# Optimization experiments

Hardware: AMD Instinct MI355X
Metric: run time of the kernel (lower is better)

Reference implementation:

```python
import math
import jax, jax.numpy as jnp
import numpy as np

DIM = 2048
NUM_HEADS = 16
HEAD_DIM = 128
SEQ = 2048
BATCH = 2
HIDDEN = 5632  # round_up(int(4*2048*2/3), 256)
EPS = 1e-6


def setup_inputs() -> dict:
    key = jax.random.key(0)
    ks = jax.random.split(key, 8)
    s = 0.02
    x = jax.random.normal(ks[0], (BATCH, SEQ, DIM), jnp.float32)
    wq = jax.random.normal(ks[1], (DIM, NUM_HEADS * HEAD_DIM), jnp.float32) * s
    wk = jax.random.normal(ks[2], (DIM, NUM_HEADS * HEAD_DIM), jnp.float32) * s
    wv = jax.random.normal(ks[3], (DIM, NUM_HEADS * HEAD_DIM), jnp.float32) * s
    wo = jax.random.normal(ks[4], (NUM_HEADS * HEAD_DIM, DIM), jnp.float32) * s
    w_mlp = jax.random.normal(ks[5], (HIDDEN, DIM), jnp.float32) * s
    v_mlp = jax.random.normal(ks[6], (HIDDEN, DIM), jnp.float32) * s
    w2_mlp = jax.random.normal(ks[7], (DIM, HIDDEN), jnp.float32) * s
    norm1_w = jnp.ones((DIM,), jnp.float32)
    norm2_w = jnp.ones((DIM,), jnp.float32)
    # RoPE tables: theta_i = 10000^{-2i/head_dim}, angle[p,i] = p * theta_i
    inv_freq = 1.0 / (10000.0 ** (np.arange(0, HEAD_DIM, 2, dtype=np.float32) / HEAD_DIM))
    angles = np.arange(SEQ, dtype=np.float32)[:, None] * inv_freq[None, :]  # [S, D/2]
    freqs_cos = jnp.asarray(np.cos(angles))
    freqs_sin = jnp.asarray(np.sin(angles))
    return {"x": x, "wq": wq, "wk": wk, "wv": wv, "wo": wo,
            "w_mlp": w_mlp, "v_mlp": v_mlp, "w2_mlp": w2_mlp,
            "norm1_w": norm1_w, "norm2_w": norm2_w,
            "freqs_cos": freqs_cos, "freqs_sin": freqs_sin}


def _rope(t, cos, sin):
    # t: [B,S,H,D] -> pairs, complex multiply by (cos + i sin)
    B, S, H, D = t.shape
    t = t.reshape(B, S, H, D // 2, 2)
    x0, x1 = t[..., 0], t[..., 1]
    c = cos[None, :S, None, :]
    s = sin[None, :S, None, :]
    o0 = x0 * c - x1 * s
    o1 = x0 * s + x1 * c
    return jnp.stack([o0, o1], axis=-1).reshape(B, S, H, D)


def _rmsnorm(x, w):
    x = x * jax.lax.rsqrt(jnp.mean(x * x, axis=-1, keepdims=True) + EPS)
    return w * x


def _attention(x, wq, wk, wv, wo, cos, sin):
    B, S, _ = x.shape
    q = (x @ wq).reshape(B, S, NUM_HEADS, HEAD_DIM)
    k = (x @ wk).reshape(B, S, NUM_HEADS, HEAD_DIM)
    v = (x @ wv).reshape(B, S, NUM_HEADS, HEAD_DIM)
    q = _rope(q, cos, sin)
    k = _rope(k, cos, sin)
    scores = jnp.einsum('bqhd,bkhd->bhqk', q, k) / math.sqrt(HEAD_DIM)
    causal = jnp.tril(jnp.ones((S, S), bool))
    scores = jnp.where(causal[None, None], scores, -jnp.inf)
    probs = jax.nn.softmax(scores.astype(jnp.float32), axis=-1)
    o = jnp.einsum('bhqk,bkhd->bqhd', probs, v).reshape(B, S, NUM_HEADS * HEAD_DIM)
    return o @ wo


def _mlp(x, w, v, w2):
    return (jax.nn.silu(x @ w.T) * (x @ v.T)) @ w2.T


def reference(x, wq, wk, wv, wo, w_mlp, v_mlp, w2_mlp, norm1_w, norm2_w, freqs_cos, freqs_sin):
    x = x + _attention(x, wq, wk, wv, wo, freqs_cos, freqs_sin)
    x = _rmsnorm(x, norm1_w)
    x = x + _mlp(x, w_mlp, v_mlp, w2_mlp)
    x = _rmsnorm(x, norm2_w)
    return x
```

## Files before the change

### kernel.cpp

```cpp
#include <hip/hip_runtime.h>

typedef unsigned short u16;
typedef unsigned int u32;
typedef float f32x4 __attribute__((ext_vector_type(4)));
typedef short bf16x8 __attribute__((ext_vector_type(8)));

#define DIM 2048
#define SEQ 2048
#define NHEAD 16
#define HDIM 128
#define BATCH 2
#define HIDDEN 5632
#define ROWS 4096

__device__ __forceinline__ float b2f(u16 h) { return __uint_as_float(((u32)h) << 16); }
__device__ __forceinline__ u16 f2b(float f) {
  u32 u = __float_as_uint(f);
  return (u16)((u + 0x7fffu + ((u >> 16) & 1u)) >> 16);
}

__global__ __launch_bounds__(256) void cvt_f2b(const float* __restrict__ in, u16* __restrict__ out, int n) {
  int i = (blockIdx.x * 256 + threadIdx.x) * 4;
  if (i < n) {
    float4 v = *(const float4*)(in + i);
    u32 p0 = (u32)f2b(v.x) | ((u32)f2b(v.y) << 16);
    u32 p1 = (u32)f2b(v.z) | ((u32)f2b(v.w) << 16);
    *(uint2*)(out + i) = make_uint2(p0, p1);
  }
}

__global__ __launch_bounds__(256) void cvtT(const float* __restrict__ in, u16* __restrict__ out,
                                            int Rr, int Cc) {
  __shared__ float t[32][33];
  int tx = threadIdx.x & 31, ty = threadIdx.x >> 5;
  int r0 = blockIdx.y * 32, c0 = blockIdx.x * 32;
#pragma unroll
  for (int rr = 0; rr < 4; ++rr)
    t[ty + rr * 8][tx] = in[(size_t)(r0 + ty + rr * 8) * Cc + c0 + tx];
  __syncthreads();
#pragma unroll
  for (int rr = 0; rr < 4; ++rr)
    out[(size_t)(c0 + ty + rr * 8) * Rr + r0 + tx] = f2b(t[tx][ty + rr * 8]);
}

__device__ __forceinline__ void stage_tile(u16* lds, const u16* __restrict__ g,
                                           int row0, int col0, int ld, int wave, int lane) {
#pragma unroll
  for (int j = 0; j < 2; ++j) {
    int i = wave * 2 + j;
    const u16* gp = g + (size_t)(row0 + i * 16 + (lane >> 2)) * ld + col0 + (lane & 3) * 8;
    __builtin_amdgcn_global_load_lds((const __attribute__((address_space(1))) void*)gp,
                                     (__attribute__((address_space(3))) void*)(lds + i * 512),
                                     16, 0, 0);
  }
}

template <int EPI>
__global__ __launch_bounds__(256) void gemm_bt(const u16* __restrict__ A, const u16* __restrict__ Bt,
                                               const void* R_, void* C_, int M, int N, int K) {
  __shared__ u16 lA[2][4096];
  __shared__ u16 lB[2][4096];
  const int tid = threadIdx.x, lane = tid & 63, wave = tid >> 6;
  const int wm = wave >> 1, wn = wave & 1;
  const int gx = gridDim.x;
  const int nwg = gx * gridDim.y;
  const int id = blockIdx.y * gx + blockIdx.x;
  const int cpx = nwg >> 3;
  const int sw = (id & 7) * cpx + (id >> 3);
  const int m0 = (sw / gx) * 128, n0 = (sw % gx) * 128;
  const int rl = lane & 15, g = lane >> 4;

  stage_tile(lA[0], A, m0, 0, K, wave, lane);
  stage_tile(lB[0], Bt, n0, 0, K, wave, lane);

  f32x4 acc[4][4];
#pragma unroll
  for (int a = 0; a < 4; ++a)
#pragma unroll
    for (int b = 0; b < 4; ++b) acc[a][b] = (f32x4){0.f, 0.f, 0.f, 0.f};

  __syncthreads();

  const int nk = K / 32;
  for (int kt = 0; kt < nk; ++kt) {
    const int cur = kt & 1;
    if (kt + 1 < nk) {
      stage_tile(lA[cur ^ 1], A, m0, (kt + 1) * 32, K, wave, lane);
      stage_tile(lB[cur ^ 1], Bt, n0, (kt + 1) * 32, K, wave, lane);
    }
    bf16x8 af[4], bfr[4];
#pragma unroll
    for (int mi = 0; mi < 4; ++mi)
      af[mi] = *reinterpret_cast<const bf16x8*>(&lA[cur][(wm * 64 + mi * 16 + rl) * 32 + g * 8]);
#pragma unroll
    for (int ni = 0; ni < 4; ++ni)
      bfr[ni] = *reinterpret_cast<const bf16x8*>(&lB[cur][(wn * 64 + ni * 16 + rl) * 32 + g * 8]);
#pragma unroll
    for (int mi = 0; mi < 4; ++mi)
#pragma unroll
      for (int ni = 0; ni < 4; ++ni)
        acc[mi][ni] = __builtin_amdgcn_mfma_f32_16x16x32_bf16(af[mi], bfr[ni], acc[mi][ni], 0, 0, 0);
    __syncthreads();
  }

#pragma unroll
  for (int mi = 0; mi < 4; ++mi)
#pragma unroll
    for (int ni = 0; ni < 4; ++ni)
#pragma unroll
      for (int j = 0; j < 4; ++j) {
        size_t row = m0 + wm * 64 + mi * 16 + g * 4 + j;
        size_t col = n0 + wn * 64 + ni * 16 + rl;
        size_t idx = row * N + col;
        float v = acc[mi][ni][j];
        if (EPI == 0) {
          ((u16*)C_)[idx] = f2b(v);
        } else if (EPI == 1) {
          ((float*)C_)[idx] = v + ((const float*)R_)[idx];
        } else if (EPI == 2) {
          float av = b2f(((const u16*)R_)[idx]);
          ((u16*)C_)[idx] = f2b(v * av / (1.f + __expf(-av)));
        } else if (EPI == 3) {
          ((float*)C_)[idx] = v + b2f(((const u16*)R_)[idx]);
        } else {
          size_t di = (col >> 11) * (size_t)(ROWS * (size_t)DIM) + row * DIM + (col & (DIM - 1));
          ((u16*)C_)[di] = f2b(v);
        }
      }
}

__global__ __launch_bounds__(256) void vtrans(const u16* __restrict__ V, u16* __restrict__ Vt) {
  __shared__ u16 t[32][33];
  int tx = threadIdx.x & 31, ty = threadIdx.x >> 5;
  int s0 = blockIdx.x * 32, d0 = blockIdx.y * 32;
  int bh = blockIdx.z, b = bh >> 4, h = bh & 15;
#pragma unroll
  for (int rr = 0; rr < 4; ++rr)
    t[ty + rr * 8][tx] = V[(size_t)(b * SEQ + s0 + ty + rr * 8) * DIM + h * HDIM + d0 + tx];
  __syncthreads();
#pragma unroll
  for (int rr = 0; rr < 4; ++rr)
    Vt[(size_t)(bh * HDIM + d0 + ty + rr * 8) * SEQ + s0 + tx] = t[tx][ty + rr * 8];
}

__global__ __launch_bounds__(256) void rope_kernel(u16* __restrict__ Q, u16* __restrict__ Kv,
                                                   const float* __restrict__ Cz, const float* __restrict__ Sz) {
  int t = blockIdx.x * 256 + threadIdx.x;
  int i = t & 63;
  int hh = (t >> 6) & 15;
  int row = t >> 10;
  int s = row & (SEQ - 1);
  float c = Cz[s * 64 + i], sn = Sz[s * 64 + i];
  size_t off = (size_t)row * DIM + hh * HDIM + 2 * i;
  const float sc = 0.08838834764831843f;

  u32 qp = *(const u32*)(Q + off);
  float q0 = b2f((u16)qp), q1 = b2f((u16)(qp >> 16));
  float o0 = (q0 * c - q1 * sn) * sc, o1 = (q0 * sn + q1 * c) * sc;
  *(u32*)(Q + off) = (u32)f2b(o0) | ((u32)f2b(o1) << 16);

  u32 kp = *(const u32*)(Kv + off);
  float k0 = b2f((u16)kp), k1 = b2f((u16)(kp >> 16));
  o0 = k0 * c - k1 * sn; o1 = k0 * sn + k1 * c;
  *(u32*)(Kv + off) = (u32)f2b(o0) | ((u32)f2b(o1) << 16);
}

__device__ __forceinline__ void stage_K(u16* lk, const u16* __restrict__ Kg,
                                        int b, int h, int t, int w, int lane) {
  const int r4 = lane >> 2;
  const int gsw = (lane & 3) ^ (r4 & 3);
#pragma unroll
  for (int j = 0; j < 4; ++j) {
    const u16* gp = Kg + (size_t)(b * SEQ + t * 64 + j * 16 + r4) * DIM +
                    h * HDIM + w * 32 + gsw * 8;
    __builtin_amdgcn_global_load_lds((const __attribute__((address_space(1))) void*)gp,
                                     (__attribute__((address_space(3))) void*)(lk + w * 2048 + j * 512),
                                     16, 0, 0);
  }
}

__device__ __forceinline__ void stage_V(u16* lv, const u16* __restrict__ Vg,
                                        int bh, int t, int w, int lane) {
  const int r4 = lane >> 2;
  const int gsw = (lane & 3) ^ (r4 & 3);
#pragma unroll
  for (int j = 0; j < 4; ++j) {
    int id = w * 4 + j, kc2 = id >> 3, rg = id & 7;
    const u16* gp = Vg + (size_t)(bh * HDIM + rg * 16 + r4) * SEQ +
                    t * 64 + kc2 * 32 + gsw * 8;
    __builtin_amdgcn_global_load_lds((const __attribute__((address_space(1))) void*)gp,
                                     (__attribute__((address_space(3))) void*)(lv + kc2 * 4096 + rg * 512),
                                     16, 0, 0);
  }
}

__global__ __launch_bounds__(256, 3) void attn_kernel(const u16* __restrict__ Q, const u16* __restrict__ Kp,
                                                      const u16* __restrict__ Vt, u16* __restrict__ O) {
  const int lane = threadIdx.x & 63;
  const int w = threadIdx.x >> 6;
  const int id = blockIdx.y * 32 + blockIdx.x;
  const int sw = (id & 7) * 128 + (id >> 3);
  const int qt = sw & 31;
  const int bh = sw >> 5;
  const int b = bh >> 4, h = bh & 15;
  const int rl = lane & 15, g = lane >> 4;
  const int gx8 = (g ^ (rl & 3)) * 8;

  __shared__ u16 lK[8192];
  __shared__ u16 lV[8192];
  __shared__ u16 plds[4][16][72];

  const size_t qrow = (size_t)b * SEQ + qt * 64 + w * 16;
  bf16x8 qf[4];
#pragma unroll
  for (int kc = 0; kc < 4; ++kc)
    qf[kc] = *reinterpret_cast<const bf16x8*>(Q + (qrow + rl) * DIM + h * HDIM + kc * 32 + g * 8);

  float m[4], l[4];
  f32x4 oacc[8];
#pragma unroll
  for (int j = 0; j < 4; ++j) { m[j] = -1e30f; l[j] = 0.f; }
#pragma unroll
  for (int dt = 0; dt < 8; ++dt) oacc[dt] = (f32x4){0.f, 0.f, 0.f, 0.f};

  const int qg0 = qt * 64 + w * 16 + g * 4;
  const int tmax = qt;

  stage_K(lK, Kp, b, h, 0, w, lane);
  stage_V(lV, Vt, bh, 0, w, lane);

  for (int t = 0; t <= tmax; ++t) {
    asm volatile("s_waitcnt vmcnt(4)" ::: "memory");
    __builtin_amdgcn_s_barrier();
    __builtin_amdgcn_sched_barrier(0);

    f32x4 s[4];
#pragma unroll
    for (int ct = 0; ct < 4; ++ct) s[ct] = (f32x4){0.f, 0.f, 0.f, 0.f};
#pragma unroll
    for (int ct = 0; ct < 4; ++ct)
#pragma unroll
      for (int kc = 0; kc < 4; ++kc) {
        bf16x8 kf = *reinterpret_cast<const bf16x8*>(&lK[kc * 2048 + (ct * 16 + rl) * 32 + gx8]);
        s[ct] = __builtin_amdgcn_mfma_f32_16x16x32_bf16(qf[kc], kf, s[ct], 0, 0, 0);
      }
    asm volatile("s_waitcnt lgkmcnt(0)" ::: "memory");
    __builtin_amdgcn_sched_barrier(0);
    __builtin_amdgcn_s_barrier();

    if (t < tmax) stage_K(lK, Kp, b, h, t + 1, w, lane);

    if (t < tmax) asm volatile("s_waitcnt vmcnt(4)" ::: "memory");
    else          asm volatile("s_waitcnt vmcnt(0)" ::: "memory");
    __builtin_amdgcn_s_barrier();
    __builtin_amdgcn_sched_barrier(0);

    if (t == qt) {
#pragma unroll
      for (int ct = 0; ct < 4; ++ct) {
        int kg = t * 64 + ct * 16 + rl;
#pragma unroll
        for (int j = 0; j < 4; ++j)
          if (kg > qg0 + j) s[ct][j] = -1e30f;
      }
    }
    float mx[4], al[4];
#pragma unroll
    for (int j = 0; j < 4; ++j)
      mx[j] = fmaxf(fmaxf(s[0][j], s[1][j]), fmaxf(s[2][j], s[3][j]));
#pragma unroll
    for (int off = 1; off < 16; off <<= 1)
#pragma unroll
      for (int j = 0; j < 4; ++j) mx[j] = fmaxf(mx[j], __shfl_xor(mx[j], off));
#pragma unroll
    for (int j = 0; j < 4; ++j) {
      float mn = fmaxf(m[j], mx[j]);
      al[j] = __expf(m[j] - mn);
      m[j] = mn;
    }
    float rs[4] = {0.f, 0.f, 0.f, 0.f};
#pragma unroll
    for (int ct = 0; ct < 4; ++ct)
#pragma unroll
      for (int j = 0; j < 4; ++j) {
        float p = __expf(s[ct][j] - m[j]);
        s[ct][j] = p;
        rs[j] += p;
      }
#pragma unroll
    for (int off = 1; off < 16; off <<= 1)
#pragma unroll
      for (int j = 0; j < 4; ++j) rs[j] += __shfl_xor(rs[j], off);
#pragma unroll
    for (int j = 0; j < 4; ++j) l[j] = l[j] * al[j] + rs[j];
#pragma unroll
    for (int dt = 0; dt < 8; ++dt)
#pragma unroll
      for (int j = 0; j < 4; ++j) oacc[dt][j] *= al[j];

#pragma unroll
    for (int ct = 0; ct < 4; ++ct)
#pragma unroll
      for (int j = 0; j < 4; ++j) plds[w][g * 4 + j][ct * 16 + rl] = f2b(s[ct][j]);

    bf16x8 pa[2];
#pragma unroll
    for (int kc2 = 0; kc2 < 2; ++kc2)
      pa[kc2] = *reinterpret_cast<const bf16x8*>(&plds[w][rl][kc2 * 32 + g * 8]);

#pragma unroll
    for (int dt = 0; dt < 8; ++dt)
#pragma unroll
      for (int kc2 = 0; kc2 < 2; ++kc2) {
        bf16x8 vf = *reinterpret_cast<const bf16x8*>(&lV[kc2 * 4096 + (dt * 16 + rl) * 32 + gx8]);
        oacc[dt] = __builtin_amdgcn_mfma_f32_16x16x32_bf16(pa[kc2], vf, oacc[dt], 0, 0, 0);
      }

    asm volatile("s_waitcnt lgkmcnt(0)" ::: "memory");
    __builtin_amdgcn_sched_barrier(0);
    __builtin_amdgcn_s_barrier();

    if (t < tmax) stage_V(lV, Vt, bh, t + 1, w, lane);
  }

  float inv[4];
#pragma unroll
  for (int j = 0; j < 4; ++j) inv[j] = 1.f / l[j];
#pragma unroll
  for (int dt = 0; dt < 8; ++dt)
#pragma unroll
    for (int j = 0; j < 4; ++j)
      O[(qrow + g * 4 + j) * DIM + h * HDIM + dt * 16 + rl] = f2b(oacc[dt][j] * inv[j]);
}

__global__ __launch_bounds__(256) void rmsnorm_to_bf16(const float* __restrict__ X, const float* __restrict__ W,
                                                       u16* __restrict__ O) {
  int row = blockIdx.x, tid = threadIdx.x;
  const float* xr = X + (size_t)row * DIM + tid * 8;
  float4 a = *(const float4*)xr;
  float4 bq = *(const float4*)(xr + 4);
  float v[8] = {a.x, a.y, a.z, a.w, bq.x, bq.y, bq.z, bq.w};
  float ss = 0.f;
#pragma unroll
  for (int j = 0; j < 8; ++j) ss += v[j] * v[j];
#pragma unroll
  for (int off = 32; off; off >>= 1) ss += __shfl_xor(ss, off);
  __shared__ float wss[4];
  int wave = tid >> 6, lane = tid & 63;
  if (lane == 0) wss[wave] = ss;
  __syncthreads();
  float r = rsqrtf((wss[0] + wss[1] + wss[2] + wss[3]) * (1.f / DIM) + 1e-6f);
  float4 wa = *(const float4*)(W + tid * 8);
  float4 wb = *(const float4*)(W + tid * 8 + 4);
  float wv[8] = {wa.x, wa.y, wa.z, wa.w, wb.x, wb.y, wb.z, wb.w};
  uint4 ou;
  ou.x = (u32)f2b(v[0] * r * wv[0]) | ((u32)f2b(v[1] * r * wv[1]) << 16);
  ou.y = (u32)f2b(v[2] * r * wv[2]) | ((u32)f2b(v[3] * r * wv[3]) << 16);
  ou.z = (u32)f2b(v[4] * r * wv[4]) | ((u32)f2b(v[5] * r * wv[5]) << 16);
  ou.w = (u32)f2b(v[6] * r * wv[6]) | ((u32)f2b(v[7] * r * wv[7]) << 16);
  *(uint4*)(O + (size_t)row * DIM + tid * 8) = ou;
}

__global__ __launch_bounds__(256) void rmsnorm_to_f32(const float* __restrict__ X, const float* __restrict__ W,
                                                      float* __restrict__ O) {
  int row = blockIdx.x, tid = threadIdx.x;
  const float* xr = X + (size_t)row * DIM + tid * 8;
  float4 a = *(const float4*)xr;
  float4 bq = *(const float4*)(xr + 4);
  float v[8] = {a.x, a.y, a.z, a.w, bq.x, bq.y, bq.z, bq.w};
  float ss = 0.f;
#pragma unroll
  for (int j = 0; j < 8; ++j) ss += v[j] * v[j];
#pragma unroll
  for (int off = 32; off; off >>= 1) ss += __shfl_xor(ss, off);
  __shared__ float wss[4];
  int wave = tid >> 6, lane = tid & 63;
  if (lane == 0) wss[wave] = ss;
  __syncthreads();
  float r = rsqrtf((wss[0] + wss[1] + wss[2] + wss[3]) * (1.f / DIM) + 1e-6f);
  float4 wa = *(const float4*)(W + tid * 8);
  float4 wb = *(const float4*)(W + tid * 8 + 4);
  float wv[8] = {wa.x, wa.y, wa.z, wa.w, wb.x, wb.y, wb.z, wb.w};
  float4 o0 = {v[0] * r * wv[0], v[1] * r * wv[1], v[2] * r * wv[2], v[3] * r * wv[3]};
  float4 o1 = {v[4] * r * wv[4], v[5] * r * wv[5], v[6] * r * wv[6], v[7] * r * wv[7]};
  *(float4*)(O + (size_t)row * DIM + tid * 8) = o0;
  *(float4*)(O + (size_t)row * DIM + tid * 8 + 4) = o1;
}

extern "C" void kernel_launch(void* const* d_in, const int* in_sizes, int n_in,
                              void* d_out, int out_size, void* d_ws, size_t ws_size,
                              hipStream_t stream) {
  const float* x     = (const float*)d_in[0];
  const float* wq    = (const float*)d_in[1];
  const float* wk    = (const float*)d_in[2];
  const float* wv    = (const float*)d_in[3];
  const float* wo    = (const float*)d_in[4];
  const float* w_mlp = (const float*)d_in[5];
  const float* v_mlp = (const float*)d_in[6];
  const float* w2    = (const float*)d_in[7];
  const float* n1w   = (const float*)d_in[8];
  const float* n2w   = (const float*)d_in[9];
  const float* fcos  = (const float*)d_in[10];
  const float* fsin  = (const float*)d_in[11];

  u16* ws = (u16*)d_ws;
  const size_t SZ = (size_t)ROWS * DIM;
  const size_t DD = (size_t)DIM * DIM;
  const size_t DH = (size_t)DIM * HIDDEN;

  u16* xb  = ws;
  u16* q   = ws + SZ;
  u16* k   = ws + 2 * SZ;
  u16* v   = ws + 3 * SZ;
  u16* vt  = ws + 4 * SZ;
  u16* hb  = ws + 5 * SZ;
  u16* W   = ws + 6 * SZ;
  u16* wqT = W;
  u16* wkT = W + DD;
  u16* wvT = W + 2 * DD;
  u16* woT = W + 3 * DD;
  u16* wmb = W;
  u16* vmb = W + DH;
  u16* w2b = W;
  float* x1f = (float*)ws;
  float* x2f = (float*)ws;
  u16* ba  = ws + 2 * SZ;

  dim3 blk(256);

  cvt_f2b<<<(int)(SZ / 4 / 256), blk, 0, stream>>>(x, xb, (int)SZ);
  dim3 gT(DIM / 32, DIM / 32);
  cvtT<<<gT, blk, 0, stream>>>(wq, wqT, DIM, DIM);
  cvtT<<<gT, blk, 0, stream>>>(wk, wkT, DIM, DIM);
  cvtT<<<gT, blk, 0, stream>>>(wv, wvT, DIM, DIM);
  cvtT<<<gT, blk, 0, stream>>>(wo, woT, DIM, DIM);

  dim3 gQKV(3 * DIM / 128, ROWS / 128);
  gemm_bt<4><<<gQKV, blk, 0, stream>>>(xb, W, nullptr, q, ROWS, 3 * DIM, DIM);

  cvt_f2b<<<(int)(DH / 4 / 256), blk, 0, stream>>>(w_mlp, wmb, (int)DH);

  rope_kernel<<<(ROWS * NHEAD * 64) / 256, blk, 0, stream>>>(q, k, fcos, fsin);
  vtrans<<<dim3(SEQ / 32, HDIM / 32, BATCH * NHEAD), blk, 0, stream>>>(v, vt);

  attn_kernel<<<dim3(SEQ / 64, BATCH * NHEAD), blk, 0, stream>>>(q, k, vt, v);

  dim3 gP(DIM / 128, ROWS / 128);
  gemm_bt<1><<<gP, blk, 0, stream>>>(v, woT, x, x1f, ROWS, DIM, DIM);

  cvt_f2b<<<(int)(DH / 4 / 256), blk, 0, stream>>>(v_mlp, vmb, (int)DH);

  rmsnorm_to_bf16<<<ROWS, blk, 0, stream>>>(x1f, n1w, hb);

  dim3 gM1(HIDDEN / 128, ROWS / 128);
  gemm_bt<0><<<gM1, blk, 0, stream>>>(hb, wmb, nullptr, ba, ROWS, HIDDEN, DIM);
  gemm_bt<2><<<gM1, blk, 0, stream>>>(hb, vmb, ba, ba, ROWS, HIDDEN, DIM);

  cvt_f2b<<<(int)(DH / 4 / 256), blk, 0, stream>>>(w2, w2b, (int)DH);

  gemm_bt<3><<<gP, blk, 0, stream>>>(ba, w2b, hb, x2f, ROWS, DIM, HIDDEN);
  rmsnorm_to_f32<<<ROWS, blk, 0, stream>>>(x2f, n2w, (float*)d_out);
}
```

Before: 813.8 us.

## Replace GEMM with 8-wave 128x256 tile kernel using phased LDS pipelining

Swaps the 4-wave 128x128 GEMM with BK=32 for an 8-wave kernel computing 128x256 tiles with BK=64. Loads are interleaved across MFMA phases with explicit vmcnt waits, barriers and setprio, so global-to-LDS staging overlaps compute. LDS addressing is XOR-swizzled to avoid bank conflicts. It uses more LDS and registers per block and relies on hand-tuned waitcnt counts that must match the number of outstanding loads.

```diff
diff --git a/kernel.cpp b/kernel.cpp
--- a/kernel.cpp
+++ b/kernel.cpp
@@ -43,74 +43,106 @@
     out[(size_t)(c0 + ty + rr * 8) * Rr + r0 + tx] = f2b(t[tx][ty + rr * 8]);
 }
 
-__device__ __forceinline__ void stage_tile(u16* lds, const u16* __restrict__ g,
-                                           int row0, int col0, int ld, int wave, int lane) {
-#pragma unroll
-  for (int j = 0; j < 2; ++j) {
-    int i = wave * 2 + j;
-    const u16* gp = g + (size_t)(row0 + i * 16 + (lane >> 2)) * ld + col0 + (lane & 3) * 8;
-    __builtin_amdgcn_global_load_lds((const __attribute__((address_space(1))) void*)gp,
-                                     (__attribute__((address_space(3))) void*)(lds + i * 512),
-                                     16, 0, 0);
+template <int EPI>
+__global__ __launch_bounds__(512, 2) void gemm8p(const u16* __restrict__ A, const u16* __restrict__ Bt,
+                                                 const void* R_, void* C_, int M, int N, int K) {
+  __shared__ u16 LA[2][8192];
+  __shared__ u16 LB[2][2][8192];
+  const int tid = threadIdx.x;
+  const int lane = tid & 63, wid = tid >> 6;
+  const int wr = wid >> 2, wc = wid & 3;
+  const int rl = lane & 15, g = lane >> 4;
+  const int s2 = ((rl >> 3) & 1) << 1;
+  const int gx = gridDim.x, gy = gridDim.y;
+  const int id = blockIdx.y * gx + blockIdx.x;
+  const int cpx = (gx * gy) >> 3;
+  const int sw = (id & 7) * cpx + (id >> 3);
+  const int m0 = (sw % gy) * 128, n0 = (sw / gy) * 256;
+  const int nk = K >> 6;
+
+  const int srow = tid >> 2;
+  const int sslot = (tid & 3) ^ (((tid >> 5) & 1) << 1);
+
+  auto SHA = [&](int ks) {
+    const u16* gp = A + (size_t)(m0 + srow) * K + ks * 64 + sslot * 8;
+#pragma unroll
+    for (int kk = 0; kk < 2; ++kk)
+      __builtin_amdgcn_global_load_lds(
+          (const __attribute__((address_space(1))) void*)(gp + kk * 32),
+          (__attribute__((address_space(3))) void*)&LA[ks & 1][kk * 4096 + wid * 512], 16, 0, 0);
+  };
+  auto SHB = [&](int ks, int hf) {
+    const u16* gp = Bt + (size_t)(n0 + hf * 128 + srow) * K + ks * 64 + sslot * 8;
+#pragma unroll
+    for (int kk = 0; kk < 2; ++kk)
+      __builtin_amdgcn_global_load_lds(
+          (const __attribute__((address_space(1))) void*)(gp + kk * 32),
+          (__attribute__((address_space(3))) void*)&LB[ks & 1][hf][kk * 4096 + wid * 512], 16, 0, 0);
+  };
+
+  f32x4 acc[4][4];
+#pragma unroll
+  for (int a = 0; a < 4; ++a)
+#pragma unroll
+    for (int b = 0; b < 4; ++b) acc[a][b] = (f32x4){0.f, 0.f, 0.f, 0.f};
+  bf16x8 bf[4][2];
+
+#define PH8(kst, q, STAGE, VMN)                                                                 \
+  do {                                                                                          \
+    const int c_ = (kst) & 1;                                                                   \
+    if ((q) == 0) {                                                                             \
+      _Pragma("unroll") for (int ni = 0; ni < 4; ++ni)                                          \
+          _Pragma("unroll") for (int kk = 0; kk < 2; ++kk)                                      \
+              bf[ni][kk] = *(const bf16x8*)&LB[c_][wc >> 1]                                     \
+                  [kk * 4096 + ((wc & 1) * 64 + ni * 16 + rl) * 32 + (g ^ s2) * 8];             \
+    }                                                                                           \
+    bf16x8 af[2];                                                                               \
+    _Pragma("unroll") for (int kk = 0; kk < 2; ++kk)                                            \
+        af[kk] = *(const bf16x8*)&LA[c_]                                                        \
+            [kk * 4096 + (wr * 64 + (q) * 16 + rl) * 32 + (g ^ s2) * 8];                        \
+    STAGE;                                                                                      \
+    __builtin_amdgcn_s_barrier();                                                               \
+    asm volatile("s_waitcnt lgkmcnt(0)" ::: "memory");                                          \
+    __builtin_amdgcn_sched_barrier(0);                                                          \
+    __builtin_amdgcn_s_setprio(1);                                                              \
+    _Pragma("unroll") for (int kk = 0; kk < 2; ++kk)                                            \
+        _Pragma("unroll") for (int ni = 0; ni < 4; ++ni)                                        \
+            acc[(q)][ni] = __builtin_amdgcn_mfma_f32_16x16x32_bf16(                             \
+                af[kk], bf[ni][kk], acc[(q)][ni], 0, 0, 0);                                     \
+    __builtin_amdgcn_s_setprio(0);                                                              \
+    if ((VMN) == 4) asm volatile("s_waitcnt vmcnt(4)" ::: "memory");                            \
+    else if ((VMN) == 6) asm volatile("s_waitcnt vmcnt(6)" ::: "memory");                       \
+    else if ((VMN) == 0) asm volatile("s_waitcnt vmcnt(0)" ::: "memory");                       \
+    __builtin_amdgcn_s_barrier();                                                               \
+  } while (0)
+
+  SHB(0, 0); SHB(0, 1); SHA(0); SHB(1, 0); SHB(1, 1); SHA(1);
+  asm volatile("s_waitcnt vmcnt(6)" ::: "memory");
+  __builtin_amdgcn_s_barrier();
+
+  const int nk2 = nk >> 1;
+  for (int i = 0; i < nk2; ++i) {
+    const int k0 = 2 * i, k1 = 2 * i + 1;
+    const bool st = (k0 + 2) < nk;
+    PH8(k0, 0, , -1);
+    PH8(k0, 1, if (st) SHB(k0 + 2, 0), -1);
+    PH8(k0, 2, if (st) SHB(k0 + 2, 1), -1);
+    PH8(k0, 3, , st ? 4 : 0);
+    PH8(k1, 0, if (st) SHA(k0 + 2), -1);
+    PH8(k1, 1, if (st) SHB(k0 + 3, 0), -1);
+    PH8(k1, 2, if (st) SHB(k0 + 3, 1), -1);
+    PH8(k1, 3, if (st) SHA(k0 + 3), st ? 6 : 0);
   }
-}
-
-template <int EPI>
-__global__ __launch_bounds__(256) void gemm_bt(const u16* __restrict__ A, const u16* __restrict__ Bt,
-                                               const void* R_, void* C_, int M, int N, int K) {
-  __shared__ u16 lA[2][4096];
-  __shared__ u16 lB[2][4096];
-  const int tid = threadIdx.x, lane = tid & 63, wave = tid >> 6;
-  const int wm = wave >> 1, wn = wave & 1;
-  const int gx = gridDim.x;
-  const int nwg = gx * gridDim.y;
-  const int id = blockIdx.y * gx + blockIdx.x;
-  const int cpx = nwg >> 3;
-  const int sw = (id & 7) * cpx + (id >> 3);
-  const int m0 = (sw / gx) * 128, n0 = (sw % gx) * 128;
-  const int rl = lane & 15, g = lane >> 4;
-
-  stage_tile(lA[0], A, m0, 0, K, wave, lane);
-  stage_tile(lB[0], Bt, n0, 0, K, wave, lane);
-
-  f32x4 acc[4][4];
-#pragma unroll
-  for (int a = 0; a < 4; ++a)
-#pragma unroll
-    for (int b = 0; b < 4; ++b) acc[a][b] = (f32x4){0.f, 0.f, 0.f, 0.f};
-
-  __syncthreads();
-
-  const int nk = K / 32;
-  for (int kt = 0; kt < nk; ++kt) {
-    const int cur = kt & 1;
-    if (kt + 1 < nk) {
-      stage_tile(lA[cur ^ 1], A, m0, (kt + 1) * 32, K, wave, lane);
-      stage_tile(lB[cur ^ 1], Bt, n0, (kt + 1) * 32, K, wave, lane);
-    }
-    bf16x8 af[4], bfr[4];
-#pragma unroll
-    for (int mi = 0; mi < 4; ++mi)
-      af[mi] = *reinterpret_cast<const bf16x8*>(&lA[cur][(wm * 64 + mi * 16 + rl) * 32 + g * 8]);
+#undef PH8
+
+#pragma unroll
+  for (int mi = 0; mi < 4; ++mi)
 #pragma unroll
     for (int ni = 0; ni < 4; ++ni)
-      bfr[ni] = *reinterpret_cast<const bf16x8*>(&lB[cur][(wn * 64 + ni * 16 + rl) * 32 + g * 8]);
-#pragma unroll
-    for (int mi = 0; mi < 4; ++mi)
-#pragma unroll
-      for (int ni = 0; ni < 4; ++ni)
-        acc[mi][ni] = __builtin_amdgcn_mfma_f32_16x16x32_bf16(af[mi], bfr[ni], acc[mi][ni], 0, 0, 0);
-    __syncthreads();
-  }
-
-#pragma unroll
-  for (int mi = 0; mi < 4; ++mi)
-#pragma unroll
-    for (int ni = 0; ni < 4; ++ni)
 #pragma unroll
       for (int j = 0; j < 4; ++j) {
-        size_t row = m0 + wm * 64 + mi * 16 + g * 4 + j;
-        size_t col = n0 + wn * 64 + ni * 16 + rl;
+        size_t row = m0 + wr * 64 + mi * 16 + g * 4 + j;
+        size_t col = n0 + wc * 64 + ni * 16 + rl;
         size_t idx = row * N + col;
         float v = acc[mi][ni][j];
         if (EPI == 0) {
@@ -427,6 +459,7 @@
   u16* ba  = ws + 2 * SZ;
 
   dim3 blk(256);
+  dim3 blk8(512);
 
   cvt_f2b<<<(int)(SZ / 4 / 256), blk, 0, stream>>>(x, xb, (int)SZ);
   dim3 gT(DIM / 32, DIM / 32);
@@ -435,8 +468,8 @@
   cvtT<<<gT, blk, 0, stream>>>(wv, wvT, DIM, DIM);
   cvtT<<<gT, blk, 0, stream>>>(wo, woT, DIM, DIM);
 
-  dim3 gQKV(3 * DIM / 128, ROWS / 128);
-  gemm_bt<4><<<gQKV, blk, 0, stream>>>(xb, W, nullptr, q, ROWS, 3 * DIM, DIM);
+  dim3 gQKV(3 * DIM / 256, ROWS / 128);
+  gemm8p<4><<<gQKV, blk8, 0, stream>>>(xb, W, nullptr, q, ROWS, 3 * DIM, DIM);
 
   cvt_f2b<<<(int)(DH / 4 / 256), blk, 0, stream>>>(w_mlp, wmb, (int)DH);
 
@@ -445,19 +478,19 @@
 
   attn_kernel<<<dim3(SEQ / 64, BATCH * NHEAD), blk, 0, stream>>>(q, k, vt, v);
 
-  dim3 gP(DIM / 128, ROWS / 128);
-  gemm_bt<1><<<gP, blk, 0, stream>>>(v, woT, x, x1f, ROWS, DIM, DIM);
+  dim3 gP(DIM / 256, ROWS / 128);
+  gemm8p<1><<<gP, blk8, 0, stream>>>(v, woT, x, x1f, ROWS, DIM, DIM);
 
   cvt_f2b<<<(int)(DH / 4 / 256), blk, 0, stream>>>(v_mlp, vmb, (int)DH);
 
   rmsnorm_to_bf16<<<ROWS, blk, 0, stream>>>(x1f, n1w, hb);
 
-  dim3 gM1(HIDDEN / 128, ROWS / 128);
-  gemm_bt<0><<<gM1, blk, 0, stream>>>(hb, wmb, nullptr, ba, ROWS, HIDDEN, DIM);
-  gemm_bt<2><<<gM1, blk, 0, stream>>>(hb, vmb, ba, ba, ROWS, HIDDEN, DIM);
+  dim3 gM(HIDDEN / 256, ROWS / 128);
+  gemm8p<0><<<gM, blk8, 0, stream>>>(hb, wmb, nullptr, ba, ROWS, HIDDEN, DIM);
+  gemm8p<2><<<gM, blk8, 0, stream>>>(hb, vmb, ba, ba, ROWS, HIDDEN, DIM);
 
   cvt_f2b<<<(int)(DH / 4 / 256), blk, 0, stream>>>(w2, w2b, (int)DH);
 
-  gemm_bt<3><<<gP, blk, 0, stream>>>(ba, w2b, hb, x2f, ROWS, DIM, HIDDEN);
+  gemm8p<3><<<gP, blk8, 0, stream>>>(ba, w2b, hb, x2f, ROWS, DIM, HIDDEN);
   rmsnorm_to_f32<<<ROWS, blk, 0, stream>>>(x2f, n2w, (float*)d_out);
 }
```

New measurement: 788.9 us. 1.03x faster.

## Widen GEMM tiles to 128x256 with 8 waves and swizzled LDS layout

Applied to the files above, without the earlier changes.

Replaces the 128x128, 4-wave GEMM with a 128x256 tile computed by 8 waves (512 threads) at a launch bound of two blocks per CU. The A tile is reused across twice as many output columns, and an XOR swizzle on the LDS slot is meant to cut bank conflicts on the fragment reads. The block-id remapping is also changed to walk M first. This doubles the B staging buffer and may lower occupancy, and for N=2048 the grid shrinks to 256 blocks, which can leave CUs underused.

```diff
diff --git a/kernel.cpp b/kernel.cpp
--- a/kernel.cpp
+++ b/kernel.cpp
@@ -43,35 +43,43 @@
     out[(size_t)(c0 + ty + rr * 8) * Rr + r0 + tx] = f2b(t[tx][ty + rr * 8]);
 }
 
-__device__ __forceinline__ void stage_tile(u16* lds, const u16* __restrict__ g,
-                                           int row0, int col0, int ld, int wave, int lane) {
-#pragma unroll
-  for (int j = 0; j < 2; ++j) {
-    int i = wave * 2 + j;
-    const u16* gp = g + (size_t)(row0 + i * 16 + (lane >> 2)) * ld + col0 + (lane & 3) * 8;
+template <int EPI>
+__global__ __launch_bounds__(512, 2) void gemm_w(const u16* __restrict__ A, const u16* __restrict__ Bt,
+                                                 const void* R_, void* C_, int M, int N, int K) {
+  __shared__ u16 lA[2][4096];
+  __shared__ u16 lB[2][8192];
+  const int tid = threadIdx.x;
+  const int lane = tid & 63, wid = tid >> 6;
+  const int wr = wid >> 2, wc = wid & 3;
+  const int rl = lane & 15, g = lane >> 4;
+  const int s2 = ((rl >> 3) & 1) << 1;
+  const int gx = gridDim.x, gy = gridDim.y;
+  const int id = blockIdx.y * gx + blockIdx.x;
+  const int cpx = (gx * gy) >> 3;
+  const int sw = (id & 7) * cpx + (id >> 3);
+  const int m0 = (sw % gy) * 128, n0 = (sw / gy) * 256;
+  const int nk = K >> 5;
+
+  const int srow = tid >> 2;
+  const int sslot = (tid & 3) ^ (((tid >> 5) & 1) << 1);
+
+  auto SA = [&](int kt, int buf) {
+    const u16* gp = A + (size_t)(m0 + srow) * K + kt * 32 + sslot * 8;
     __builtin_amdgcn_global_load_lds((const __attribute__((address_space(1))) void*)gp,
-                                     (__attribute__((address_space(3))) void*)(lds + i * 512),
+                                     (__attribute__((address_space(3))) void*)&lA[buf][wid * 512],
                                      16, 0, 0);
-  }
-}
-
-template <int EPI>
-__global__ __launch_bounds__(256) void gemm_bt(const u16* __restrict__ A, const u16* __restrict__ Bt,
-                                               const void* R_, void* C_, int M, int N, int K) {
-  __shared__ u16 lA[2][4096];
-  __shared__ u16 lB[2][4096];
-  const int tid = threadIdx.x, lane = tid & 63, wave = tid >> 6;
-  const int wm = wave >> 1, wn = wave & 1;
-  const int gx = gridDim.x;
-  const int nwg = gx * gridDim.y;
-  const int id = blockIdx.y * gx + blockIdx.x;
-  const int cpx = nwg >> 3;
-  const int sw = (id & 7) * cpx + (id >> 3);
-  const int m0 = (sw / gx) * 128, n0 = (sw % gx) * 128;
-  const int rl = lane & 15, g = lane >> 4;
-
-  stage_tile(lA[0], A, m0, 0, K, wave, lane);
-  stage_tile(lB[0], Bt, n0, 0, K, wave, lane);
+  };
+  auto SB = [&](int kt, int buf) {
+#pragma unroll
+    for (int j = 0; j < 2; ++j) {
+      const u16* gp = Bt + (size_t)(n0 + j * 128 + srow) * K + kt * 32 + sslot * 8;
+      __builtin_amdgcn_global_load_lds((const __attribute__((address_space(1))) void*)gp,
+                                       (__attribute__((address_space(3))) void*)&lB[buf][j * 4096 + wid * 512],
+                                       16, 0, 0);
+    }
+  };
+
+  SA(0, 0); SB(0, 0);
 
   f32x4 acc[4][4];
 #pragma unroll
@@ -81,20 +89,16 @@
 
   __syncthreads();
 
-  const int nk = K / 32;
   for (int kt = 0; kt < nk; ++kt) {
     const int cur = kt & 1;
-    if (kt + 1 < nk) {
-      stage_tile(lA[cur ^ 1], A, m0, (kt + 1) * 32, K, wave, lane);
-      stage_tile(lB[cur ^ 1], Bt, n0, (kt + 1) * 32, K, wave, lane);
-    }
+    if (kt + 1 < nk) { SA(kt + 1, cur ^ 1); SB(kt + 1, cur ^ 1); }
     bf16x8 af[4], bfr[4];
 #pragma unroll
     for (int mi = 0; mi < 4; ++mi)
-      af[mi] = *reinterpret_cast<const bf16x8*>(&lA[cur][(wm * 64 + mi * 16 + rl) * 32 + g * 8]);
+      af[mi] = *reinterpret_cast<const bf16x8*>(&lA[cur][(wr * 64 + mi * 16 + rl) * 32 + (g ^ s2) * 8]);
 #pragma unroll
     for (int ni = 0; ni < 4; ++ni)
-      bfr[ni] = *reinterpret_cast<const bf16x8*>(&lB[cur][(wn * 64 + ni * 16 + rl) * 32 + g * 8]);
+      bfr[ni] = *reinterpret_cast<const bf16x8*>(&lB[cur][(wc * 64 + ni * 16 + rl) * 32 + (g ^ s2) * 8]);
 #pragma unroll
     for (int mi = 0; mi < 4; ++mi)
 #pragma unroll
@@ -109,8 +113,8 @@
     for (int ni = 0; ni < 4; ++ni)
 #pragma unroll
       for (int j = 0; j < 4; ++j) {
-        size_t row = m0 + wm * 64 + mi * 16 + g * 4 + j;
-        size_t col = n0 + wn * 64 + ni * 16 + rl;
+        size_t row = m0 + wr * 64 + mi * 16 + g * 4 + j;
+        size_t col = n0 + wc * 64 + ni * 16 + rl;
         size_t idx = row * N + col;
         float v = acc[mi][ni][j];
         if (EPI == 0) {
@@ -427,6 +431,7 @@
   u16* ba  = ws + 2 * SZ;
 
   dim3 blk(256);
+  dim3 blk8(512);
 
   cvt_f2b<<<(int)(SZ / 4 / 256), blk, 0, stream>>>(x, xb, (int)SZ);
   dim3 gT(DIM / 32, DIM / 32);
@@ -435,8 +440,8 @@
   cvtT<<<gT, blk, 0, stream>>>(wv, wvT, DIM, DIM);
   cvtT<<<gT, blk, 0, stream>>>(wo, woT, DIM, DIM);
 
-  dim3 gQKV(3 * DIM / 128, ROWS / 128);
-  gemm_bt<4><<<gQKV, blk, 0, stream>>>(xb, W, nullptr, q, ROWS, 3 * DIM, DIM);
+  dim3 gQKV(3 * DIM / 256, ROWS / 128);
+  gemm_w<4><<<gQKV, blk8, 0, stream>>>(xb, W, nullptr, q, ROWS, 3 * DIM, DIM);
 
   cvt_f2b<<<(int)(DH / 4 / 256), blk, 0, stream>>>(w_mlp, wmb, (int)DH);
 
@@ -445,19 +450,19 @@
 
   attn_kernel<<<dim3(SEQ / 64, BATCH * NHEAD), blk, 0, stream>>>(q, k, vt, v);
 
-  dim3 gP(DIM / 128, ROWS / 128);
-  gemm_bt<1><<<gP, blk, 0, stream>>>(v, woT, x, x1f, ROWS, DIM, DIM);
+  dim3 gP(DIM / 256, ROWS / 128);
+  gemm_w<1><<<gP, blk8, 0, stream>>>(v, woT, x, x1f, ROWS, DIM, DIM);
 
   cvt_f2b<<<(int)(DH / 4 / 256), blk, 0, stream>>>(v_mlp, vmb, (int)DH);
 
   rmsnorm_to_bf16<<<ROWS, blk, 0, stream>>>(x1f, n1w, hb);
 
-  dim3 gM1(HIDDEN / 128, ROWS / 128);
-  gemm_bt<0><<<gM1, blk, 0, stream>>>(hb, wmb, nullptr, ba, ROWS, HIDDEN, DIM);
-  gemm_bt<2><<<gM1, blk, 0, stream>>>(hb, vmb, ba, ba, ROWS, HIDDEN, DIM);
+  dim3 gM(HIDDEN / 256, ROWS / 128);
+  gemm_w<0><<<gM, blk8, 0, stream>>>(hb, wmb, nullptr, ba, ROWS, HIDDEN, DIM);
+  gemm_w<2><<<gM, blk8, 0, stream>>>(hb, vmb, ba, ba, ROWS, HIDDEN, DIM);
 
   cvt_f2b<<<(int)(DH / 4 / 256), blk, 0, stream>>>(w2, w2b, (int)DH);
 
-  gemm_bt<3><<<gP, blk, 0, stream>>>(ba, w2b, hb, x2f, ROWS, DIM, HIDDEN);
+  gemm_w<3><<<gP, blk8, 0, stream>>>(ba, w2b, hb, x2f, ROWS, DIM, HIDDEN);
   rmsnorm_to_f32<<<ROWS, blk, 0, stream>>>(x2f, n2w, (float*)d_out);
 }
```

Result: slower. 870.9 us (+7.0%).
